# Kernel tuning notes

Measured on AMD Instinct MI355X. Metric: run time of the kernel, lower is better.

## Reference

```python
import jax, jax.numpy as jnp
import numpy as np

B, C, H, W = 8, 64, 256, 256
N_HEADS = 4
MODES_X, MODES_Y = 32, 32 // 2 + 1  # rfft half-spectrum along last dim
O_PER_HEAD = C // N_HEADS


def setup_inputs() -> dict:
    key = jax.random.key(0)
    k1, k2, k3 = jax.random.split(key, 3)
    x = jax.random.normal(k1, (B, C, H, W), dtype=jnp.float32)
    weights_real = jax.random.normal(k2, (N_HEADS, C, O_PER_HEAD, MODES_X, MODES_Y), dtype=jnp.float32) * 0.01
    weights_imag = jax.random.normal(k3, (N_HEADS, C, O_PER_HEAD, MODES_X, MODES_Y), dtype=jnp.float32) * 0.01
    bias = jnp.zeros((C, 1, 1), dtype=jnp.float32)
    return {"x": x, "weights_real": weights_real, "weights_imag": weights_imag, "bias": bias}


def reference(x, weights_real, weights_imag, bias):
    b, c, h, w = x.shape
    nh, _, o, mxw, myw = weights_real.shape
    # rfft2 with ortho norm, matching torch.fft.rfft2(..., norm='ortho')
    xf = jnp.fft.rfft2(x, norm="ortho")  # [B, C, H, W//2+1] complex64
    fH, fW = xf.shape[-2], xf.shape[-1]
    mx = min(mxw, fH)
    my = min(myw, fW)
    wgt = weights_real[..., :mx, :my] + 1j * weights_imag[..., :mx, :my]  # [nh, C, o, mx, my]
    # all heads at once: torch loop 'biXY,ioXY->boXY' per head == 'bixy,hioxy->bhoxy'
    prod = jnp.einsum("bixy,hioxy->bhoxy", xf[:, :, :mx, :my], wgt)  # [B, nh, o, mx, my]
    out_f = jnp.zeros((b, nh, o, fH, fW), dtype=prod.dtype).at[..., :mx, :my].set(prod)
    out = jnp.fft.irfft2(out_f, s=(h, w), norm="ortho")  # [B, nh, o, H, W] real
    # torch.cat over heads along channel dim == head-major reshape
    out = out.reshape(b, nh * o, h, w)
    return out + bias  # bias [C,1,1] broadcasts
```

## Files before the change

### kernel.cpp

```cpp
#include <hip/hip_runtime.h>
#include <hip/hip_bf16.h>

#define NROWS 131072
#define MY 17
#define MX 32


#define K1_ROWS 30
#define NCHUNK 9

__global__ __launch_bounds__(512) void f1_fw(const float* __restrict__ x,
                                             float2* __restrict__ X2) {
    __shared__ __align__(16) float s_lds[4][K1_ROWS][68];
    __shared__ float2 xs[4352];
    int t = threadIdx.x;
    int bc = blockIdx.x;
    const float* xp = x + (long)bc * 65536;

    int j = t % 17;
    int r = t / 17;
    int rc = r < K1_ROWS ? r : 0;
    int odd = j & 1;
    float ca = odd ? 0.f : ((j & 2) ? -1.f : 1.f);
    float cb = odd ? (((j & 3) == 1) ? -1.f : 1.f) : 0.f;
    float cj, sj;
    sincospif((float)j * (1.0f / 128.0f), &sj, &cj);
    sj = -sj;
    float swv, cwv;
    sincospif((float)j * 0.25f, &swv, &cwv);
    swv = -swv;
    float k1c = cwv * ca - swv * cb;
    float k2c = swv * ca + cwv * cb;
    const float4* A4 = (const float4*)&s_lds[odd ? 1 : 0][rc][0];
    const float4* B4 = (const float4*)&s_lds[odd ? 3 : 2][rc][0];

    float4 q0, q1, q2, q3;

#define F1_REGLOAD(cc)                                                         \
    {                                                                          \
        int nr_ = ((cc) < 8) ? K1_ROWS : 16;                                   \
        int items_ = nr_ * 16;                                                 \
        int it = t < items_ ? t : items_ - 1;                                  \
        int rr = it >> 4, cq = it & 15;                                        \
        const float4* xr =                                                     \
            (const float4*)(xp + ((cc) * K1_ROWS + rr) * 256) + cq;            \
        q0 = xr[0];                                                            \
        q1 = xr[16];                                                           \
        q2 = xr[32];                                                           \
        q3 = xr[48];                                                           \
    }

    F1_REGLOAD(0)

    for (int c = 0; c < NCHUNK; ++c) {
        int nr = (c < 8) ? K1_ROWS : 16;
        int items = nr * 16;

        if (t < items) {
            int rr = t >> 4, cq = t & 15;
            float4 s02p, s02m, s13p, s13m;
            s02p.x = q0.x + q2.x; s02p.y = q0.y + q2.y;
            s02p.z = q0.z + q2.z; s02p.w = q0.w + q2.w;
            s02m.x = q0.x - q2.x; s02m.y = q0.y - q2.y;
            s02m.z = q0.z - q2.z; s02m.w = q0.w - q2.w;
            s13p.x = q1.x + q3.x; s13p.y = q1.y + q3.y;
            s13p.z = q1.z + q3.z; s13p.w = q1.w + q3.w;
            s13m.x = q1.x - q3.x; s13m.y = q1.y - q3.y;
            s13m.z = q1.z - q3.z; s13m.w = q1.w - q3.w;
            *(float4*)&s_lds[0][rr][cq * 4] = s02p;
            *(float4*)&s_lds[1][rr][cq * 4] = s02m;
            *(float4*)&s_lds[2][rr][cq * 4] = s13p;
            *(float4*)&s_lds[3][rr][cq * 4] = s13m;
        }
        __syncthreads();

        if (c + 1 < NCHUNK) F1_REGLOAD(c + 1)

        if (t < 510 && r < nr) {
            float pc = 1.f, ps = 0.f;
            float ar0 = 0, ai0 = 0;

#define K1_STEP(a0e, b0e, a0f, b0f)                                   \
  { float t0re = fmaf(k1c, (b0f), fmaf(cwv, (a0f), fmaf(ca, (b0e), (a0e)))); \
    float t0im = fmaf(k2c, (b0f), fmaf(swv, (a0f), cb * (b0e)));      \
    ar0 = fmaf(t0re, pc, ar0); ar0 = fmaf(-t0im, ps, ar0);            \
    ai0 = fmaf(t0re, ps, ai0); ai0 = fmaf(t0im, pc, ai0);             \
    float nps = fmaf(pc, sj, ps * cj);                                \
    pc = fmaf(pc, cj, -(ps * sj)); ps = nps; }

#pragma unroll 2
            for (int l4 = 0; l4 < 8; ++l4) {
                float4 va0 = A4[l4], vb0 = B4[l4];
                float4 vA0 = A4[8 + l4], vB0 = B4[8 + l4];
                K1_STEP(va0.x, vb0.x, vA0.x, vB0.x)
                K1_STEP(va0.y, vb0.y, vA0.y, vB0.y)
                K1_STEP(va0.z, vb0.z, vA0.z, vB0.z)
                K1_STEP(va0.w, vb0.w, vA0.w, vB0.w)
            }
#undef K1_STEP

            int h = c * K1_ROWS + r;
            xs[h * 17 + j] = make_float2(ar0, ai0);
        }
        __syncthreads();
    }

    for (int q = t; q < 2176; q += 512) {
        float2 a = xs[q], b = xs[q + 2176];
        xs[q] = make_float2(a.x + b.x, a.y + b.y);
        xs[q + 2176] = make_float2(a.x - b.x, a.y - b.y);
    }
    __syncthreads();

    for (int q = t; q < 544; q += 512) {
        int kx = q / 17, ky = q % 17;
        int kodd = kx & 1;
        float cA = kodd ? 0.f : ((kx & 2) ? -1.f : 1.f);
        float cB = kodd ? (((kx & 3) == 1) ? -1.f : 1.f) : 0.f;
        float cBn = -cB;
        const float2* Aq = xs + (kodd ? 2176 : 0) + ky;
        float cs, ss;
        sincospif((float)kx * (1.0f / 128.0f), &ss, &cs);
        ss = -ss;
        float pc = 1.f, psn = 0.f;
        float ar = 0.f, ai = 0.f;
#pragma unroll 4
        for (int m = 0; m < 64; ++m) {
            float2 a = Aq[m * 17];
            float2 b = Aq[1088 + m * 17];
            float yre = fmaf(cBn, b.y, fmaf(cA, b.x, a.x));
            float yim = fmaf(cB, b.x, fmaf(cA, b.y, a.y));
            ar = fmaf(yre, pc, ar); ar = fmaf(-yim, psn, ar);
            ai = fmaf(yre, psn, ai); ai = fmaf(yim, pc, ai);
            float npc = pc * cs - psn * ss;
            psn = pc * ss + psn * cs;
            pc = npc;
        }
        X2[(long)bc * 544 + q] = make_float2(ar, ai);
    }
#undef F1_REGLOAD
}

__global__ __launch_bounds__(512) void f2b_inv(const float2* __restrict__ X2,
                                               const float* __restrict__ wr_g,
                                               const float* __restrict__ wi_g,
                                               const float* __restrict__ bias,
                                               float* __restrict__ out) {
    __shared__ float2 psh[544];
    __shared__ float2 zsh[4352];
    int t = threadIdx.x;
    int plane = blockIdx.x;
    int b = plane >> 6;
    int ho = plane & 63;
    int n = ho >> 4;
    int o = ho & 15;

    for (int q = t; q < 544; q += 512) {
        const float2* xp = X2 + (long)b * 64 * 544 + q;
        const float* wrp = wr_g + ((long)(n * 64) * 16 + o) * 544 + q;
        const float* wip = wi_g + ((long)(n * 64) * 16 + o) * 544 + q;
        float ar = 0.f, ai = 0.f;
#pragma unroll 4
        for (int i = 0; i < 64; ++i) {
            float2 xv = xp[i * 544];
            float wvr = wrp[i * 8704];
            float wvi = wip[i * 8704];
            ar += xv.x * wvr - xv.y * wvi;
            ai += xv.x * wvi + xv.y * wvr;
        }
        psh[q] = make_float2(ar, ai);
    }
    __syncthreads();

    {
        int h = t & 255;
        int half = t >> 8;
        int kyb = half ? 9 : 0;
        int cnt = half ? 8 : 9;
        float chh, shh;
        sincospif((float)h * (1.0f / 128.0f), &shh, &chh);
        float pc = 1.f, psn = 0.f;
        float ar[9], ai[9];
#pragma unroll
        for (int u = 0; u < 9; ++u) { ar[u] = 0.f; ai[u] = 0.f; }

        const float2* pq = psh + kyb;
        for (int kx = 0; kx < 32; ++kx) {
#pragma unroll
            for (int u = 0; u < 9; ++u) {
                if (u < cnt) {
                    float2 v = pq[kx * 17 + u];
                    ar[u] += v.x * pc - v.y * psn;
                    ai[u] += v.x * psn + v.y * pc;
                }
            }
            float npc = pc * chh - psn * shh;
            psn = pc * shh + psn * chh;
            pc = npc;
        }
#pragma unroll
        for (int u = 0; u < 9; ++u)
            if (u < cnt) zsh[h * 17 + kyb + u] = make_float2(ar[u], ai[u]);
    }
    __syncthreads();

    int wv = t >> 6;
    int lane = t & 63;
    float bv = bias[plane & 63];
    float c0, s0;
    sincospif((float)lane * (1.0f / 128.0f), &s0, &c0);
    const float inv = 1.0f / 65536.0f;
    const float inv2 = 2.0f / 65536.0f;
    long ob_plane = (long)plane * 65536;

    for (int it16 = 0; it16 < 16; ++it16) {
        int r0 = it16 * 16 + wv * 2;
        float pc = c0, psn = s0;
        float a00 = 0, a01 = 0, a02 = 0, a03 = 0;
        float a10 = 0, a11 = 0, a12 = 0, a13 = 0;

#pragma unroll
        for (int ky = 1; ky <= 16; ++ky) {
            float2 z0 = zsh[r0 * 17 + ky];
            float2 z1 = zsh[(r0 + 1) * 17 + ky];
            float A0 = z0.x * pc - z0.y * psn;
            float B0 = z0.x * psn + z0.y * pc;
            float A1 = z1.x * pc - z1.y * psn;
            float B1 = z1.x * psn + z1.y * pc;
            a00 += A0; a10 += A1;
            a01 += ((ky & 3) == 0) ? A0 : ((ky & 3) == 1) ? -B0 : ((ky & 3) == 2) ? -A0 : B0;
            a11 += ((ky & 3) == 0) ? A1 : ((ky & 3) == 1) ? -B1 : ((ky & 3) == 2) ? -A1 : B1;
            a02 += (ky & 1) ? -A0 : A0;
            a12 += (ky & 1) ? -A1 : A1;
            a03 += ((ky & 3) == 0) ? A0 : ((ky & 3) == 1) ? B0 : ((ky & 3) == 2) ? -A0 : -B0;
            a13 += ((ky & 3) == 0) ? A1 : ((ky & 3) == 1) ? B1 : ((ky & 3) == 2) ? -A1 : -B1;
            float npc = pc * c0 - psn * s0;
            psn = pc * s0 + psn * c0;
            pc = npc;
        }
        float base0 = zsh[r0 * 17].x * inv + bv;
        float base1 = zsh[(r0 + 1) * 17].x * inv + bv;
        long ob0 = ob_plane + (long)r0 * 256;
        long ob1 = ob0 + 256;
        out[ob0 + lane]       = fmaf(a00, inv2, base0);
        out[ob0 + 64 + lane]  = fmaf(a01, inv2, base0);
        out[ob0 + 128 + lane] = fmaf(a02, inv2, base0);
        out[ob0 + 192 + lane] = fmaf(a03, inv2, base0);
        out[ob1 + lane]       = fmaf(a10, inv2, base1);
        out[ob1 + 64 + lane]  = fmaf(a11, inv2, base1);
        out[ob1 + 128 + lane] = fmaf(a12, inv2, base1);
        out[ob1 + 192 + lane] = fmaf(a13, inv2, base1);
    }
}

extern "C" void kernel_launch(void* const* d_in, const int* in_sizes, int n_in,
                              void* d_out, int out_size, void* d_ws, size_t ws_size,
                              hipStream_t stream) {
    const float* x = (const float*)d_in[0];
    const float* wr = (const float*)d_in[1];
    const float* wi = (const float*)d_in[2];
    const float* bias = (const float*)d_in[3];
    float* out = (float*)d_out;
    float* ws = (float*)d_ws;

    float2* X2 = (float2*)(ws + 4456960);

    hipLaunchKernelGGL(f1_fw, dim3(512), dim3(512), 0, stream, x, X2);
    hipLaunchKernelGGL(f2b_inv, dim3(512), dim3(512), 0, stream, X2, wr, wi, bias, out);
}
```

Baseline: 121.1 us.

## Split inverse kernel so final row-iDFT runs as separate fine-grained launch

The fused inverse kernel is split in two. k_ab does the spectral mixing and the column inverse DFT per plane and writes the intermediate Z to a global workspace. A new k_c kernel uses 4096 blocks of 256 threads, each handling 32 rows of a plane, to run the final real inverse along the rows plus bias and write the output. The aim is to raise occupancy and spread the write-heavy last stage across many more blocks. The cost is an extra kernel launch and a global round-trip of the roughly 18 MB intermediate.

Measured after the change: 127.1 us. 1.05x slower.

```diff
diff --git a/kernel.cpp b/kernel.cpp
--- a/kernel.cpp
+++ b/kernel.cpp
@@ -141,13 +141,11 @@
 #undef F1_REGLOAD
 }
 
-__global__ __launch_bounds__(512) void f2b_inv(const float2* __restrict__ X2,
-                                               const float* __restrict__ wr_g,
-                                               const float* __restrict__ wi_g,
-                                               const float* __restrict__ bias,
-                                               float* __restrict__ out) {
+__global__ __launch_bounds__(512) void k_ab(const float2* __restrict__ X2,
+                                            const float* __restrict__ wr_g,
+                                            const float* __restrict__ wi_g,
+                                            float2* __restrict__ Z) {
     __shared__ float2 psh[544];
-    __shared__ float2 zsh[4352];
     int t = threadIdx.x;
     int plane = blockIdx.x;
     int b = plane >> 6;
@@ -198,9 +196,26 @@
             psn = pc * shh + psn * chh;
             pc = npc;
         }
+        float2* zp = Z + (long)plane * 4352 + h;
 #pragma unroll
         for (int u = 0; u < 9; ++u)
-            if (u < cnt) zsh[h * 17 + kyb + u] = make_float2(ar[u], ai[u]);
+            if (u < cnt) zp[(kyb + u) * 256] = make_float2(ar[u], ai[u]);
+    }
+}
+
+__global__ __launch_bounds__(256) void k_c(const float2* __restrict__ Z,
+                                           const float* __restrict__ bias,
+                                           float* __restrict__ out) {
+    __shared__ float2 zsl[544];
+    int t = threadIdx.x;
+    int bi = blockIdx.x;
+    int plane = bi >> 3;
+    int base = (bi & 7) * 32;
+    const float2* zp = Z + (long)plane * 4352;
+
+    for (int q = t; q < 544; q += 256) {
+        int ky = q >> 5, r = q & 31;
+        zsl[r * 17 + ky] = zp[ky * 256 + base + r];
     }
     __syncthreads();
 
@@ -211,18 +226,18 @@
     sincospif((float)lane * (1.0f / 128.0f), &s0, &c0);
     const float inv = 1.0f / 65536.0f;
     const float inv2 = 2.0f / 65536.0f;
-    long ob_plane = (long)plane * 65536;
-
-    for (int it16 = 0; it16 < 16; ++it16) {
-        int r0 = it16 * 16 + wv * 2;
+    long ob_plane = (long)plane * 65536 + (long)base * 256;
+
+    for (int it = 0; it < 4; ++it) {
+        int r0 = it * 8 + wv * 2;
         float pc = c0, psn = s0;
         float a00 = 0, a01 = 0, a02 = 0, a03 = 0;
         float a10 = 0, a11 = 0, a12 = 0, a13 = 0;
 
 #pragma unroll
         for (int ky = 1; ky <= 16; ++ky) {
-            float2 z0 = zsh[r0 * 17 + ky];
-            float2 z1 = zsh[(r0 + 1) * 17 + ky];
+            float2 z0 = zsl[r0 * 17 + ky];
+            float2 z1 = zsl[(r0 + 1) * 17 + ky];
             float A0 = z0.x * pc - z0.y * psn;
             float B0 = z0.x * psn + z0.y * pc;
             float A1 = z1.x * pc - z1.y * psn;
@@ -238,8 +253,8 @@
             psn = pc * s0 + psn * c0;
             pc = npc;
         }
-        float base0 = zsh[r0 * 17].x * inv + bv;
-        float base1 = zsh[(r0 + 1) * 17].x * inv + bv;
+        float base0 = zsl[r0 * 17].x * inv + bv;
+        float base1 = zsl[(r0 + 1) * 17].x * inv + bv;
         long ob0 = ob_plane + (long)r0 * 256;
         long ob1 = ob0 + 256;
         out[ob0 + lane]       = fmaf(a00, inv2, base0);
@@ -263,8 +278,10 @@
     float* out = (float*)d_out;
     float* ws = (float*)d_ws;
 
+    float2* Z  = (float2*)(ws + 512);
     float2* X2 = (float2*)(ws + 4456960);
 
     hipLaunchKernelGGL(f1_fw, dim3(512), dim3(512), 0, stream, x, X2);
-    hipLaunchKernelGGL(f2b_inv, dim3(512), dim3(512), 0, stream, X2, wr, wi, bias, out);
-}
+    hipLaunchKernelGGL(k_ab, dim3(512), dim3(512), 0, stream, X2, wr, wi, Z);
+    hipLaunchKernelGGL(k_c, dim3(4096), dim3(256), 0, stream, Z, bias, out);
+}
```

## Use even/odd butterfly splits in inverse DFT stages to halve twiddle work

Applied to the files above, without the earlier changes.

The column inverse DFT now splits the kx sum into even and odd parts, so each thread computes rows h and h+128 together through a butterfly. The 128 threads per group each cover a smaller set of ky. The final row inverse DFT pre-combines ky and ky+8 pairs with a per-lane twiddle and uses precomputed twiddle arrays, which halves the inner multiply count and removes the serial recurrence. This trades fewer FLOPs for more registers and slightly different rounding.

Measured after the change: 115.1 us. -4.9%, faster.

```diff
diff --git a/kernel.cpp b/kernel.cpp
--- a/kernel.cpp
+++ b/kernel.cpp
@@ -141,7 +141,7 @@
 #undef F1_REGLOAD
 }
 
-__global__ __launch_bounds__(512) void f2b_inv(const float2* __restrict__ X2,
+__global__ __launch_bounds__(512) void f2c_inv(const float2* __restrict__ X2,
                                                const float* __restrict__ wr_g,
                                                const float* __restrict__ wi_g,
                                                const float* __restrict__ bias,
@@ -173,25 +173,31 @@
     __syncthreads();
 
     {
-        int h = t & 255;
-        int half = t >> 8;
-        int kyb = half ? 9 : 0;
-        int cnt = half ? 8 : 9;
+        int h = t & 127;
+        int grp = t >> 7;
+        int kyb = (grp == 0) ? 0 : (4 * grp + 1);
+        int cnt = (grp == 0) ? 5 : 4;
         float chh, shh;
         sincospif((float)h * (1.0f / 128.0f), &shh, &chh);
         float pc = 1.f, psn = 0.f;
-        float ar[9], ai[9];
-#pragma unroll
-        for (int u = 0; u < 9; ++u) { ar[u] = 0.f; ai[u] = 0.f; }
+        float aer[5], aei[5], aor[5], aoi[5];
+#pragma unroll
+        for (int u = 0; u < 5; ++u) { aer[u] = 0.f; aei[u] = 0.f; aor[u] = 0.f; aoi[u] = 0.f; }
 
         const float2* pq = psh + kyb;
+#pragma unroll
         for (int kx = 0; kx < 32; ++kx) {
 #pragma unroll
-            for (int u = 0; u < 9; ++u) {
+            for (int u = 0; u < 5; ++u) {
                 if (u < cnt) {
                     float2 v = pq[kx * 17 + u];
-                    ar[u] += v.x * pc - v.y * psn;
-                    ai[u] += v.x * psn + v.y * pc;
+                    if ((kx & 1) == 0) {
+                        aer[u] = fmaf(v.x, pc, fmaf(-v.y, psn, aer[u]));
+                        aei[u] = fmaf(v.x, psn, fmaf(v.y, pc, aei[u]));
+                    } else {
+                        aor[u] = fmaf(v.x, pc, fmaf(-v.y, psn, aor[u]));
+                        aoi[u] = fmaf(v.x, psn, fmaf(v.y, pc, aoi[u]));
+                    }
                 }
             }
             float npc = pc * chh - psn * shh;
@@ -199,8 +205,13 @@
             pc = npc;
         }
 #pragma unroll
-        for (int u = 0; u < 9; ++u)
-            if (u < cnt) zsh[h * 17 + kyb + u] = make_float2(ar[u], ai[u]);
+        for (int u = 0; u < 5; ++u) {
+            if (u < cnt) {
+                int ky = kyb + u;
+                zsh[h * 17 + ky] = make_float2(aer[u] + aor[u], aei[u] + aoi[u]);
+                zsh[(h + 128) * 17 + ky] = make_float2(aer[u] - aor[u], aei[u] - aoi[u]);
+            }
+        }
     }
     __syncthreads();
 
@@ -209,24 +220,51 @@
     float bv = bias[plane & 63];
     float c0, s0;
     sincospif((float)lane * (1.0f / 128.0f), &s0, &c0);
+    float c8, s8;
+    sincospif((float)lane * (1.0f / 16.0f), &s8, &c8);
+
+    float pcv[8], psv[8];
+    {
+        float pc = c0, ps = s0;
+#pragma unroll
+        for (int k = 0; k < 8; ++k) {
+            pcv[k] = pc; psv[k] = ps;
+            float nps = fmaf(pc, s0, ps * c0);
+            pc = fmaf(pc, c0, -(ps * s0));
+            ps = nps;
+        }
+    }
+
     const float inv = 1.0f / 65536.0f;
     const float inv2 = 2.0f / 65536.0f;
     long ob_plane = (long)plane * 65536;
 
     for (int it16 = 0; it16 < 16; ++it16) {
         int r0 = it16 * 16 + wv * 2;
-        float pc = c0, psn = s0;
+
+        float zz0r[8], zz0i[8], zz1r[8], zz1i[8];
+#pragma unroll
+        for (int k = 0; k < 8; ++k) {
+            int ky = k + 1;
+            float2 a0 = zsh[r0 * 17 + ky];
+            float2 b0 = zsh[r0 * 17 + ky + 8];
+            float2 a1 = zsh[(r0 + 1) * 17 + ky];
+            float2 b1 = zsh[(r0 + 1) * 17 + ky + 8];
+            zz0r[k] = fmaf(b0.x, c8, fmaf(-b0.y, s8, a0.x));
+            zz0i[k] = fmaf(b0.x, s8, fmaf(b0.y, c8, a0.y));
+            zz1r[k] = fmaf(b1.x, c8, fmaf(-b1.y, s8, a1.x));
+            zz1i[k] = fmaf(b1.x, s8, fmaf(b1.y, c8, a1.y));
+        }
+
         float a00 = 0, a01 = 0, a02 = 0, a03 = 0;
         float a10 = 0, a11 = 0, a12 = 0, a13 = 0;
-
-#pragma unroll
-        for (int ky = 1; ky <= 16; ++ky) {
-            float2 z0 = zsh[r0 * 17 + ky];
-            float2 z1 = zsh[(r0 + 1) * 17 + ky];
-            float A0 = z0.x * pc - z0.y * psn;
-            float B0 = z0.x * psn + z0.y * pc;
-            float A1 = z1.x * pc - z1.y * psn;
-            float B1 = z1.x * psn + z1.y * pc;
+#pragma unroll
+        for (int k = 0; k < 8; ++k) {
+            int ky = k + 1;
+            float A0 = zz0r[k] * pcv[k] - zz0i[k] * psv[k];
+            float B0 = zz0r[k] * psv[k] + zz0i[k] * pcv[k];
+            float A1 = zz1r[k] * pcv[k] - zz1i[k] * psv[k];
+            float B1 = zz1r[k] * psv[k] + zz1i[k] * pcv[k];
             a00 += A0; a10 += A1;
             a01 += ((ky & 3) == 0) ? A0 : ((ky & 3) == 1) ? -B0 : ((ky & 3) == 2) ? -A0 : B0;
             a11 += ((ky & 3) == 0) ? A1 : ((ky & 3) == 1) ? -B1 : ((ky & 3) == 2) ? -A1 : B1;
@@ -234,9 +272,6 @@
             a12 += (ky & 1) ? -A1 : A1;
             a03 += ((ky & 3) == 0) ? A0 : ((ky & 3) == 1) ? B0 : ((ky & 3) == 2) ? -A0 : -B0;
             a13 += ((ky & 3) == 0) ? A1 : ((ky & 3) == 1) ? B1 : ((ky & 3) == 2) ? -A1 : -B1;
-            float npc = pc * c0 - psn * s0;
-            psn = pc * s0 + psn * c0;
-            pc = npc;
         }
         float base0 = zsh[r0 * 17].x * inv + bv;
         float base1 = zsh[(r0 + 1) * 17].x * inv + bv;
@@ -266,5 +301,5 @@
     float2* X2 = (float2*)(ws + 4456960);
 
     hipLaunchKernelGGL(f1_fw, dim3(512), dim3(512), 0, stream, x, X2);
-    hipLaunchKernelGGL(f2b_inv, dim3(512), dim3(512), 0, stream, X2, wr, wi, bias, out);
+    hipLaunchKernelGGL(f2c_inv, dim3(512), dim3(512), 0, stream, X2, wr, wi, bias, out);
 }
```
